# Kernel tuning notes

Measured on AMD Instinct MI355X. Metric: run time of the kernel, lower is better.

The kernel has to match this reference:

```python
import jax, jax.numpy as jnp
import numpy as np
from jax import lax

NEG_INF = -10000.0  # matches the torch code's fill value


def setup_inputs() -> dict:
    key = jax.random.key(0)
    k1, k2, k3 = jax.random.split(key, 3)
    B, T, L = 512, 512, 102  # n_labels = vocab_size(100) + 2
    logits = jax.random.normal(k1, (B, T, L), dtype=jnp.float32)
    transitions = jax.random.normal(k2, (L, L), dtype=jnp.float32)
    lens = jax.random.randint(k3, (B,), 0, 512, dtype=jnp.int32)
    return {"logits": logits, "transitions": transitions, "lens": lens}


def reference(logits, transitions, lens):
    """Linear-chain CRF partition function (forward algorithm).

    logits: [B, T, L] emission scores (L = n_labels incl. start/stop)
    transitions: [L, L], transitions[j, k] = score of k -> j
    lens: [B] int sequence lengths
    returns: [B] log partition function
    """
    B, T, L = logits.shape
    start_idx, stop_idx = L - 2, L - 1

    alpha0 = jnp.full((B, L), NEG_INF, dtype=logits.dtype).at[:, start_idx].set(0.0)

    def step(carry, logit_t):
        alpha, c_lens = carry  # alpha: [B, L], logit_t: [B, L]
        # mat[b, j, k] = transitions[j, k] + alpha[b, k]
        mat = transitions[None, :, :] + alpha[:, None, :]
        alpha_nxt = logit_t + jax.scipy.special.logsumexp(mat, axis=2)  # [B, L]
        alive = (c_lens > 0)[:, None]
        alpha = jnp.where(alive, alpha_nxt, alpha)
        return (alpha, c_lens - 1), None

    (alpha, _), _ = lax.scan(step, (alpha0, lens), jnp.swapaxes(logits, 0, 1))

    alpha = alpha + transitions[stop_idx][None, :]
    norm = jax.scipy.special.logsumexp(alpha, axis=1)  # [B]
    return norm
```

## Files before the change

### kernel.cpp

```cpp
#include <hip/hip_runtime.h>


typedef _Float16 half2_t __attribute__((ext_vector_type(2)));

#define CRF_L 102
#define CRF_RP 104
#define CRF_START 100
#define CRF_STOP 101
#define NEG_BIG (-1.0e30f)
#define LN2F 0.6931471805599453f

#define REP13(X) X(0) X(1) X(2) X(3) X(4) X(5) X(6) X(7) X(8) X(9) X(10) X(11) X(12)

#define FDOT2(a, b, c) __builtin_amdgcn_fdot2((a), (b), (c), false)

template <int CTRL>
__device__ __forceinline__ float dpp_add_step(float x) {
    int xi = __builtin_bit_cast(int, x);
    int yi = __builtin_amdgcn_update_dpp(0, xi, CTRL, 0xf, 0xf, true);
    return x + __builtin_bit_cast(float, yi);
}
__device__ __forceinline__ float wave_sum64(float v) {
    v = dpp_add_step<0x111>(v);
    v = dpp_add_step<0x112>(v);
    v = dpp_add_step<0x114>(v);
    v = dpp_add_step<0x118>(v);
    v = dpp_add_step<0x142>(v);
    v = dpp_add_step<0x143>(v);
    return __builtin_bit_cast(float,
        __builtin_amdgcn_readlane(__builtin_bit_cast(int, v), 63));
}

__device__ __forceinline__ half2_t mk2(const float* rowp, int k, float rmx) {
    float e0 = (k + 0 < CRF_L) ? __expf(rowp[k + 0] - rmx) : 0.f;
    float e1 = (k + 1 < CRF_L) ? __expf(rowp[k + 1] - rmx) : 0.f;
    return (half2_t){(_Float16)e0, (_Float16)e1};
}

__attribute__((amdgpu_waves_per_eu(1, 1)))
__launch_bounds__(64)
__global__ void crf_forward_kernel(const float* __restrict__ logits,
                                   const float* __restrict__ trans,
                                   const int* __restrict__ lens,
                                   float* __restrict__ out,
                                   int B, int T) {
    const int b    = blockIdx.x;
    const int lane = threadIdx.x;
    const int r0   = 2 * lane;
    const int r1   = 2 * lane + 1;
    const bool valid = (lane < 51);

    __shared__ __align__(16) float TS[CRF_L * CRF_RP];
    __shared__ __align__(16) _Float16 Q[112];

    #pragma unroll 4
    for (int r = 0; r < CRF_L; ++r)
        for (int c = lane; c < CRF_L; c += 64)
            TS[CRF_RP * r + c] = trans[CRF_L * r + c];

    if (lane < 56) {
        int i0 = 2 * lane;
        Q[i0]     = (_Float16)((i0 == CRF_START) ? 1.f : 0.f);
        Q[i0 + 1] = (_Float16)0.f;
    }
    __builtin_amdgcn_wave_barrier();

    const float* rowA = &TS[CRF_RP * (valid ? r0 : 0)];
    const float* rowB = &TS[CRF_RP * (valid ? r1 : 0)];
    float rmax0 = NEG_BIG, rmax1 = NEG_BIG;
    #pragma unroll
    for (int k = 0; k < CRF_L; ++k) {
        rmax0 = fmaxf(rmax0, rowA[k]);
        rmax1 = fmaxf(rmax1, rowB[k]);
    }

#define DECLM(j) half2_t ma##j##_0, ma##j##_1, ma##j##_2, ma##j##_3, \
                         mb##j##_0, mb##j##_1, mb##j##_2, mb##j##_3;
    REP13(DECLM)
#undef DECLM
#define PACKJ(j) \
    ma##j##_0 = mk2(rowA, 8*(j)+0, rmax0); ma##j##_1 = mk2(rowA, 8*(j)+2, rmax0); \
    ma##j##_2 = mk2(rowA, 8*(j)+4, rmax0); ma##j##_3 = mk2(rowA, 8*(j)+6, rmax0); \
    mb##j##_0 = mk2(rowB, 8*(j)+0, rmax1); mb##j##_1 = mk2(rowB, 8*(j)+2, rmax1); \
    mb##j##_2 = mk2(rowB, 8*(j)+4, rmax1); mb##j##_3 = mk2(rowB, 8*(j)+6, rmax1);
    REP13(PACKJ)
#undef PACKJ

    const float erm0 = (valid)              ? rmax0 : NEG_BIG;
    const float erm1 = (valid && r1 < CRF_L) ? rmax1 : NEG_BIG;

    const int len = min(lens[b], T);
    const float* lg = logits + (size_t)b * (size_t)T * (size_t)CRF_L;
    const int loff = valid ? r0 : 0;

    float2 l0 = *reinterpret_cast<const float2*>(lg + loff);
    float2 lgB = *reinterpret_cast<const float2*>(lg + (size_t)min(1, T - 1) * CRF_L + loff);
    float2 lgC = *reinterpret_cast<const float2*>(lg + (size_t)min(2, T - 1) * CRF_L + loff);
    float2 Ec = make_float2(__expf(l0.x + erm0), __expf(l0.y + erm1));

    float invRs = 0.00390625f;
    float log2Rs = 0.f;
    float Lacc = 0.f;
    float q0 = 0.f, q1 = 0.f;
    const int sidx = min(r0, 102);

    for (int t = 0; t < len; ++t) {
        const float4* P4 = reinterpret_cast<const float4*>(&Q[0]);
        float c0 = 0.f, c1 = 0.f, c2 = 0.f, c3 = 0.f;
        float d0 = 0.f, d1 = 0.f, d2 = 0.f, d3 = 0.f;
#define DOT(j) { float4 q = P4[j]; \
        half2_t q0h = __builtin_bit_cast(half2_t, q.x); \
        half2_t q1h = __builtin_bit_cast(half2_t, q.y); \
        half2_t q2h = __builtin_bit_cast(half2_t, q.z); \
        half2_t q3h = __builtin_bit_cast(half2_t, q.w); \
        c0 = FDOT2(ma##j##_0, q0h, c0); c1 = FDOT2(ma##j##_1, q1h, c1); \
        c2 = FDOT2(ma##j##_2, q2h, c2); c3 = FDOT2(ma##j##_3, q3h, c3); \
        d0 = FDOT2(mb##j##_0, q0h, d0); d1 = FDOT2(mb##j##_1, q1h, d1); \
        d2 = FDOT2(mb##j##_2, q2h, d2); d3 = FDOT2(mb##j##_3, q3h, d3); }
        REP13(DOT)
#undef DOT
        float dot0 = (c0 + c1) + (c2 + c3);
        float dot1 = (d0 + d1) + (d2 + d3);

        Lacc += log2Rs + 8.0f;
        q0 = (dot0 * Ec.x) * invRs;
        q1 = (dot1 * Ec.y) * invRs;

        __builtin_amdgcn_wave_barrier();
        *reinterpret_cast<half2_t*>(&Q[sidx]) =
            (half2_t){(_Float16)q0, (_Float16)q1};
        __builtin_amdgcn_wave_barrier();

        float R = wave_sum64(q0 + q1);
        R = fmaxf(R, 1e-30f);
        invRs = __builtin_amdgcn_rcpf(R) * 0.00390625f;
        log2Rs = __log2f(R);

        Ec.x = __expf(lgB.x + erm0);
        Ec.y = __expf(lgB.y + erm1);
        lgB = lgC;
        lgC = *reinterpret_cast<const float2*>(lg + (size_t)min(t + 3, T - 1) * CRF_L + loff);
    }

    float ts0 = TS[CRF_RP * CRF_STOP + (valid ? r0 : 0)];
    float ts1 = TS[CRF_RP * CRF_STOP + (valid ? r1 : 0)];
    float e;
    if (len == 0) {
        e = ((r0 == CRF_START) ? __expf(ts0) : 0.f);
    } else {
        e = q0 * __expf(ts0) + q1 * __expf(ts1);
    }
    float se = wave_sum64(e);

    if (lane == 0) out[b] = LN2F * Lacc + __logf(se);
}

extern "C" void kernel_launch(void* const* d_in, const int* in_sizes, int n_in,
                              void* d_out, int out_size, void* d_ws, size_t ws_size,
                              hipStream_t stream) {
    const float* logits = (const float*)d_in[0];
    const float* trans  = (const float*)d_in[1];
    const int*   lens   = (const int*)d_in[2];
    float* out = (float*)d_out;

    const int B = 512;
    const int T = 512;

    crf_forward_kernel<<<dim3(B), dim3(64), 0, stream>>>(
        logits, trans, lens, out, B, T);
}
```

Before: 410.8 us.

## Broadcast alpha via readlane instead of LDS round-trip in CRF forward loop

Replaces the per-step write of packed half2 alpha into shared memory, and the following float4 reads, with 51 scalar readlanes from a register that holds each lane's packed value. The wave barriers and LDS latency on the serial time recurrence go away, but each step now issues 51 v_readlane instructions that become SGPR operands to the fdot2 ops. It also folds the 1/R normalization into the emission factor ahead of time, removing a multiply from the critical path. The per-pair weight registers are reorganized to one pair per readlane.

```diff
diff --git a/kernel.cpp b/kernel.cpp
--- a/kernel.cpp
+++ b/kernel.cpp
@@ -10,7 +10,26 @@
 #define NEG_BIG (-1.0e30f)
 #define LN2F 0.6931471805599453f
 
-#define REP13(X) X(0) X(1) X(2) X(3) X(4) X(5) X(6) X(7) X(8) X(9) X(10) X(11) X(12)
+#define REP51(X) X(0) X(1) X(2) X(3) X(4) X(5) X(6) X(7) X(8) X(9) \
+                 X(10) X(11) X(12) X(13) X(14) X(15) X(16) X(17) X(18) X(19) \
+                 X(20) X(21) X(22) X(23) X(24) X(25) X(26) X(27) X(28) X(29) \
+                 X(30) X(31) X(32) X(33) X(34) X(35) X(36) X(37) X(38) X(39) \
+                 X(40) X(41) X(42) X(43) X(44) X(45) X(46) X(47) X(48) X(49) X(50)
+
+#define DOT_ALL(X) \
+    X(0,c0,d0)  X(1,c1,d1)  X(2,c2,d2)  X(3,c3,d3) \
+    X(4,c0,d0)  X(5,c1,d1)  X(6,c2,d2)  X(7,c3,d3) \
+    X(8,c0,d0)  X(9,c1,d1)  X(10,c2,d2) X(11,c3,d3) \
+    X(12,c0,d0) X(13,c1,d1) X(14,c2,d2) X(15,c3,d3) \
+    X(16,c0,d0) X(17,c1,d1) X(18,c2,d2) X(19,c3,d3) \
+    X(20,c0,d0) X(21,c1,d1) X(22,c2,d2) X(23,c3,d3) \
+    X(24,c0,d0) X(25,c1,d1) X(26,c2,d2) X(27,c3,d3) \
+    X(28,c0,d0) X(29,c1,d1) X(30,c2,d2) X(31,c3,d3) \
+    X(32,c0,d0) X(33,c1,d1) X(34,c2,d2) X(35,c3,d3) \
+    X(36,c0,d0) X(37,c1,d1) X(38,c2,d2) X(39,c3,d3) \
+    X(40,c0,d0) X(41,c1,d1) X(42,c2,d2) X(43,c3,d3) \
+    X(44,c0,d0) X(45,c1,d1) X(46,c2,d2) X(47,c3,d3) \
+    X(48,c0,d0) X(49,c1,d1) X(50,c2,d2)
 
 #define FDOT2(a, b, c) __builtin_amdgcn_fdot2((a), (b), (c), false)
 
@@ -32,8 +51,8 @@
 }
 
 __device__ __forceinline__ half2_t mk2(const float* rowp, int k, float rmx) {
-    float e0 = (k + 0 < CRF_L) ? __expf(rowp[k + 0] - rmx) : 0.f;
-    float e1 = (k + 1 < CRF_L) ? __expf(rowp[k + 1] - rmx) : 0.f;
+    float e0 = __expf(rowp[k + 0] - rmx);
+    float e1 = __expf(rowp[k + 1] - rmx);
     return (half2_t){(_Float16)e0, (_Float16)e1};
 }
 
@@ -51,18 +70,11 @@
     const bool valid = (lane < 51);
 
     __shared__ __align__(16) float TS[CRF_L * CRF_RP];
-    __shared__ __align__(16) _Float16 Q[112];
 
     #pragma unroll 4
     for (int r = 0; r < CRF_L; ++r)
         for (int c = lane; c < CRF_L; c += 64)
             TS[CRF_RP * r + c] = trans[CRF_L * r + c];
-
-    if (lane < 56) {
-        int i0 = 2 * lane;
-        Q[i0]     = (_Float16)((i0 == CRF_START) ? 1.f : 0.f);
-        Q[i0 + 1] = (_Float16)0.f;
-    }
     __builtin_amdgcn_wave_barrier();
 
     const float* rowA = &TS[CRF_RP * (valid ? r0 : 0)];
@@ -74,70 +86,62 @@
         rmax1 = fmaxf(rmax1, rowB[k]);
     }
 
-#define DECLM(j) half2_t ma##j##_0, ma##j##_1, ma##j##_2, ma##j##_3, \
-                         mb##j##_0, mb##j##_1, mb##j##_2, mb##j##_3;
-    REP13(DECLM)
+#define DECLM(k) half2_t ma##k, mb##k;
+    REP51(DECLM)
 #undef DECLM
-#define PACKJ(j) \
-    ma##j##_0 = mk2(rowA, 8*(j)+0, rmax0); ma##j##_1 = mk2(rowA, 8*(j)+2, rmax0); \
-    ma##j##_2 = mk2(rowA, 8*(j)+4, rmax0); ma##j##_3 = mk2(rowA, 8*(j)+6, rmax0); \
-    mb##j##_0 = mk2(rowB, 8*(j)+0, rmax1); mb##j##_1 = mk2(rowB, 8*(j)+2, rmax1); \
-    mb##j##_2 = mk2(rowB, 8*(j)+4, rmax1); mb##j##_3 = mk2(rowB, 8*(j)+6, rmax1);
-    REP13(PACKJ)
-#undef PACKJ
+#define PACKM(k) ma##k = mk2(rowA, 2*(k), rmax0); mb##k = mk2(rowB, 2*(k), rmax1);
+    REP51(PACKM)
+#undef PACKM
 
-    const float erm0 = (valid)              ? rmax0 : NEG_BIG;
-    const float erm1 = (valid && r1 < CRF_L) ? rmax1 : NEG_BIG;
+    const float erm0 = valid ? rmax0 : NEG_BIG;
+    const float erm1 = valid ? rmax1 : NEG_BIG;
 
     const int len = min(lens[b], T);
     const float* lg = logits + (size_t)b * (size_t)T * (size_t)CRF_L;
     const int loff = valid ? r0 : 0;
 
-    float2 l0 = *reinterpret_cast<const float2*>(lg + loff);
+    float2 l0  = *reinterpret_cast<const float2*>(lg + loff);
     float2 lgB = *reinterpret_cast<const float2*>(lg + (size_t)min(1, T - 1) * CRF_L + loff);
     float2 lgC = *reinterpret_cast<const float2*>(lg + (size_t)min(2, T - 1) * CRF_L + loff);
-    float2 Ec = make_float2(__expf(l0.x + erm0), __expf(l0.y + erm1));
 
-    float invRs = 0.00390625f;
+    float invRs  = 0.00390625f;
     float log2Rs = 0.f;
-    float Lacc = 0.f;
+    float Lacc   = 0.f;
+    float2 EcI = make_float2(__expf(l0.x + erm0) * invRs,
+                             __expf(l0.y + erm1) * invRs);
+
     float q0 = 0.f, q1 = 0.f;
-    const int sidx = min(r0, 102);
+    half2_t qp0 = (half2_t){(_Float16)((r0 == CRF_START) ? 1.f : 0.f),
+                            (_Float16)0.f};
+    int qbits = __builtin_bit_cast(int, qp0);
 
     for (int t = 0; t < len; ++t) {
-        const float4* P4 = reinterpret_cast<const float4*>(&Q[0]);
+#define RDL(k) int sq##k = __builtin_amdgcn_readlane(qbits, k);
+        REP51(RDL)
+#undef RDL
+
         float c0 = 0.f, c1 = 0.f, c2 = 0.f, c3 = 0.f;
         float d0 = 0.f, d1 = 0.f, d2 = 0.f, d3 = 0.f;
-#define DOT(j) { float4 q = P4[j]; \
-        half2_t q0h = __builtin_bit_cast(half2_t, q.x); \
-        half2_t q1h = __builtin_bit_cast(half2_t, q.y); \
-        half2_t q2h = __builtin_bit_cast(half2_t, q.z); \
-        half2_t q3h = __builtin_bit_cast(half2_t, q.w); \
-        c0 = FDOT2(ma##j##_0, q0h, c0); c1 = FDOT2(ma##j##_1, q1h, c1); \
-        c2 = FDOT2(ma##j##_2, q2h, c2); c3 = FDOT2(ma##j##_3, q3h, c3); \
-        d0 = FDOT2(mb##j##_0, q0h, d0); d1 = FDOT2(mb##j##_1, q1h, d1); \
-        d2 = FDOT2(mb##j##_2, q2h, d2); d3 = FDOT2(mb##j##_3, q3h, d3); }
-        REP13(DOT)
-#undef DOT
+#define DOTA(k, ci, di) { half2_t qh = __builtin_bit_cast(half2_t, sq##k); \
+        ci = FDOT2(ma##k, qh, ci); di = FDOT2(mb##k, qh, di); }
+        DOT_ALL(DOTA)
+#undef DOTA
         float dot0 = (c0 + c1) + (c2 + c3);
         float dot1 = (d0 + d1) + (d2 + d3);
 
         Lacc += log2Rs + 8.0f;
-        q0 = (dot0 * Ec.x) * invRs;
-        q1 = (dot1 * Ec.y) * invRs;
-
-        __builtin_amdgcn_wave_barrier();
-        *reinterpret_cast<half2_t*>(&Q[sidx]) =
-            (half2_t){(_Float16)q0, (_Float16)q1};
-        __builtin_amdgcn_wave_barrier();
+        q0 = dot0 * EcI.x;
+        q1 = dot1 * EcI.y;
+        half2_t qp = (half2_t){(_Float16)q0, (_Float16)q1};
+        qbits = __builtin_bit_cast(int, qp);
 
         float R = wave_sum64(q0 + q1);
         R = fmaxf(R, 1e-30f);
-        invRs = __builtin_amdgcn_rcpf(R) * 0.00390625f;
+        invRs  = __builtin_amdgcn_rcpf(R) * 0.00390625f;
         log2Rs = __log2f(R);
 
-        Ec.x = __expf(lgB.x + erm0);
-        Ec.y = __expf(lgB.y + erm1);
+        EcI.x = __expf(lgB.x + erm0) * invRs;
+        EcI.y = __expf(lgB.y + erm1) * invRs;
         lgB = lgC;
         lgC = *reinterpret_cast<const float2*>(lg + (size_t)min(t + 3, T - 1) * CRF_L + loff);
     }
```

New measurement: 443.3 us. 7.9% more time.
